# Performance work log

Hardware: AMD Instinct MI355X
Metric: run time of the kernel (lower is better)

Reference implementation:

```python
import jax, jax.numpy as jnp
import numpy as np

B, C, H, W, K = 32, 256, 56, 56, 4


def setup_inputs() -> dict:
    key = jax.random.key(0)
    k0, k1, k2, k3, k4 = jax.random.split(key, 5)
    return {
        "x0": jax.random.normal(k0, (B, C, H, W), dtype=jnp.float32),
        "x1": jax.random.normal(k1, (B, C, H, W), dtype=jnp.float32),
        "x2": jax.random.normal(k2, (B, C, H, W), dtype=jnp.float32),
        "x3": jax.random.normal(k3, (B, C, H, W), dtype=jnp.float32),
        "attn_logits": jax.random.normal(k4, (K, B, C), dtype=jnp.float32),
    }


def reference(x0, x1, x2, x3, attn_logits):
    # Stack K branches: [K, B, C, H, W]
    xs = jnp.stack([x0, x1, x2, x3], axis=0)
    # Op (1): U = sum over branches, S = global average pool over H,W -> [B, C]
    u = xs.sum(axis=0)                      # [B, C, H, W]
    s = u.mean(axis=(2, 3))                 # [B, C]
    # Op (2): per-(b,c) softmax over the K branch logits, then weighted fuse
    w = jax.nn.softmax(attn_logits, axis=0)  # [K, B, C]
    out = jnp.einsum("kbc,kbchw->bchw", w, xs)  # [B, C, H, W]
    # u_sum (HW-sum of U) as written by the fused kernel when write_usum=true
    u_sum = u.sum(axis=(2, 3))              # [B, C]
    return out, s, u_sum
```

## Files before the change

### kernel.cpp

```cpp
#include <hip/hip_runtime.h>

constexpr int B = 32, C = 256, H = 56, W = 56, K = 4;
constexpr int HW = H * W;
constexpr int BC = B * C;
constexpr long long IMG = (long long)BC * HW;

typedef float f4 __attribute__((ext_vector_type(4)));

__global__ __launch_bounds__(256) void sk_fuse_kernel(
    const float* __restrict__ x0, const float* __restrict__ x1,
    const float* __restrict__ x2, const float* __restrict__ x3,
    const float* __restrict__ logits,
    float* __restrict__ out,
    float* __restrict__ s_out,
    float* __restrict__ usum_out)
{
    const int bc  = blockIdx.x;
    const int tid = threadIdx.x;

    const float l0 = logits[0 * BC + bc];
    const float l1 = logits[1 * BC + bc];
    const float l2 = logits[2 * BC + bc];
    const float l3 = logits[3 * BC + bc];
    const float m  = fmaxf(fmaxf(l0, l1), fmaxf(l2, l3));
    const float e0 = expf(l0 - m);
    const float e1 = expf(l1 - m);
    const float e2 = expf(l2 - m);
    const float e3 = expf(l3 - m);
    const float inv = 1.0f / (e0 + e1 + e2 + e3);
    const float w0 = e0 * inv, w1 = e1 * inv, w2 = e2 * inv, w3 = e3 * inv;

    const size_t base = (size_t)bc * HW;
    const f4* __restrict__ p0 = (const f4*)(x0 + base);
    const f4* __restrict__ p1 = (const f4*)(x1 + base);
    const f4* __restrict__ p2 = (const f4*)(x2 + base);
    const f4* __restrict__ p3 = (const f4*)(x3 + base);
    f4* __restrict__ po = (f4*)(out + base);

    const int i0 = tid, i1 = tid + 256, i2 = tid + 512;
    const f4 a0 = p0[i0], b0 = p1[i0], c0 = p2[i0], d0 = p3[i0];
    const f4 a1 = p0[i1], b1 = p1[i1], c1 = p2[i1], d1 = p3[i1];
    const f4 a2 = p0[i2], b2 = p1[i2], c2 = p2[i2], d2 = p3[i2];

    const bool tail = (tid < 16);
    const int i3 = 768 + (tid & 15);
    f4 a3 = 0.0f, b3 = 0.0f, c3 = 0.0f, d3 = 0.0f;
    if (tail) { a3 = p0[i3]; b3 = p1[i3]; c3 = p2[i3]; d3 = p3[i3]; }

    float usum = 0.0f;

    auto fuse = [&](const f4& a, const f4& b,
                    const f4& c, const f4& d) -> f4 {
        f4 o;
        o.x = w0 * a.x + w1 * b.x + w2 * c.x + w3 * d.x;
        o.y = w0 * a.y + w1 * b.y + w2 * c.y + w3 * d.y;
        o.z = w0 * a.z + w1 * b.z + w2 * c.z + w3 * d.z;
        o.w = w0 * a.w + w1 * b.w + w2 * c.w + w3 * d.w;
        usum += (a.x + b.x + c.x + d.x)
              + (a.y + b.y + c.y + d.y)
              + (a.z + b.z + c.z + d.z)
              + (a.w + b.w + c.w + d.w);
        return o;
    };

    {
        const f4 o = fuse(a0, b0, c0, d0);
        __builtin_nontemporal_store(o, &po[i0]);
    }
    {
        const f4 o = fuse(a1, b1, c1, d1);
        __builtin_nontemporal_store(o, &po[i1]);
    }
    {
        const f4 o = fuse(a2, b2, c2, d2);
        __builtin_nontemporal_store(o, &po[i2]);
    }
    if (tail) {
        const f4 o = fuse(a3, b3, c3, d3);
        __builtin_nontemporal_store(o, &po[i3]);
    }

    #pragma unroll
    for (int off = 32; off > 0; off >>= 1)
        usum += __shfl_down(usum, off, 64);

    __shared__ float wsum[4];
    const int lane = tid & 63;
    const int wid  = tid >> 6;
    if (lane == 0) wsum[wid] = usum;
    __syncthreads();
    if (tid == 0) {
        const float t = wsum[0] + wsum[1] + wsum[2] + wsum[3];
        usum_out[bc] = t;
        s_out[bc]    = t * (1.0f / HW);
    }
}

extern "C" void kernel_launch(void* const* d_in, const int* in_sizes, int n_in,
                              void* d_out, int out_size, void* d_ws, size_t ws_size,
                              hipStream_t stream) {
    const float* x0     = (const float*)d_in[0];
    const float* x1     = (const float*)d_in[1];
    const float* x2     = (const float*)d_in[2];
    const float* x3     = (const float*)d_in[3];
    const float* logits = (const float*)d_in[4];

    float* out      = (float*)d_out;
    float* s_out    = out + IMG;
    float* usum_out = s_out + BC;

    sk_fuse_kernel<<<BC, 256, 0, stream>>>(x0, x1, x2, x3, logits,
                                           out, s_out, usum_out);
}
```

Measured before the change: 94.41 us.

## Process four planes per block with double-buffered register prefetch

Each block now handles four (b,c) planes instead of one. The loads for the next plane are issued into a second register buffer while the current plane is fused and stored, and the four reductions share a single shared-memory pass. The aim is to keep more memory requests in flight per thread and to spread per-block setup over more work. In exchange it uses more VGPRs (two 16-f4 buffers), which may lower occupancy, and it launches only 2048 blocks.

```diff
diff --git a/kernel.cpp b/kernel.cpp
--- a/kernel.cpp
+++ b/kernel.cpp
@@ -4,8 +4,57 @@
 constexpr int HW = H * W;
 constexpr int BC = B * C;
 constexpr long long IMG = (long long)BC * HW;
+constexpr int NP = 4;
 
 typedef float f4 __attribute__((ext_vector_type(4)));
+
+struct PlaneRegs { f4 v[16]; };
+
+__device__ __forceinline__ void issue_loads(
+    PlaneRegs& R,
+    const f4* __restrict__ p0, const f4* __restrict__ p1,
+    const f4* __restrict__ p2, const f4* __restrict__ p3,
+    int i0, int i1, int i2, int i3, bool tail)
+{
+    R.v[ 0] = p0[i0]; R.v[ 1] = p1[i0]; R.v[ 2] = p2[i0]; R.v[ 3] = p3[i0];
+    R.v[ 4] = p0[i1]; R.v[ 5] = p1[i1]; R.v[ 6] = p2[i1]; R.v[ 7] = p3[i1];
+    R.v[ 8] = p0[i2]; R.v[ 9] = p1[i2]; R.v[10] = p2[i2]; R.v[11] = p3[i2];
+    if (tail) {
+        R.v[12] = p0[i3]; R.v[13] = p1[i3]; R.v[14] = p2[i3]; R.v[15] = p3[i3];
+    } else {
+        R.v[12] = 0.0f; R.v[13] = 0.0f; R.v[14] = 0.0f; R.v[15] = 0.0f;
+    }
+}
+
+__device__ __forceinline__ f4 fuse1(const f4& a, const f4& b,
+                                    const f4& c, const f4& d,
+                                    float w0, float w1, float w2, float w3,
+                                    float& usum)
+{
+    f4 o;
+    o.x = w0 * a.x + w1 * b.x + w2 * c.x + w3 * d.x;
+    o.y = w0 * a.y + w1 * b.y + w2 * c.y + w3 * d.y;
+    o.z = w0 * a.z + w1 * b.z + w2 * c.z + w3 * d.z;
+    o.w = w0 * a.w + w1 * b.w + w2 * c.w + w3 * d.w;
+    usum += (a.x + b.x + c.x + d.x)
+          + (a.y + b.y + c.y + d.y)
+          + (a.z + b.z + c.z + d.z)
+          + (a.w + b.w + c.w + d.w);
+    return o;
+}
+
+__device__ __forceinline__ float consume(
+    const PlaneRegs& R, float w0, float w1, float w2, float w3,
+    f4* __restrict__ po, int i0, int i1, int i2, int i3, bool tail)
+{
+    float us = 0.0f;
+    __builtin_nontemporal_store(fuse1(R.v[0],R.v[1],R.v[ 2],R.v[ 3],w0,w1,w2,w3,us), &po[i0]);
+    __builtin_nontemporal_store(fuse1(R.v[4],R.v[5],R.v[ 6],R.v[ 7],w0,w1,w2,w3,us), &po[i1]);
+    __builtin_nontemporal_store(fuse1(R.v[8],R.v[9],R.v[10],R.v[11],w0,w1,w2,w3,us), &po[i2]);
+    if (tail)
+        __builtin_nontemporal_store(fuse1(R.v[12],R.v[13],R.v[14],R.v[15],w0,w1,w2,w3,us), &po[i3]);
+    return us;
+}
 
 __global__ __launch_bounds__(256) void sk_fuse_kernel(
     const float* __restrict__ x0, const float* __restrict__ x1,
@@ -15,84 +64,73 @@
     float* __restrict__ s_out,
     float* __restrict__ usum_out)
 {
-    const int bc  = blockIdx.x;
     const int tid = threadIdx.x;
-
-    const float l0 = logits[0 * BC + bc];
-    const float l1 = logits[1 * BC + bc];
-    const float l2 = logits[2 * BC + bc];
-    const float l3 = logits[3 * BC + bc];
-    const float m  = fmaxf(fmaxf(l0, l1), fmaxf(l2, l3));
-    const float e0 = expf(l0 - m);
-    const float e1 = expf(l1 - m);
-    const float e2 = expf(l2 - m);
-    const float e3 = expf(l3 - m);
-    const float inv = 1.0f / (e0 + e1 + e2 + e3);
-    const float w0 = e0 * inv, w1 = e1 * inv, w2 = e2 * inv, w3 = e3 * inv;
-
-    const size_t base = (size_t)bc * HW;
-    const f4* __restrict__ p0 = (const f4*)(x0 + base);
-    const f4* __restrict__ p1 = (const f4*)(x1 + base);
-    const f4* __restrict__ p2 = (const f4*)(x2 + base);
-    const f4* __restrict__ p3 = (const f4*)(x3 + base);
-    f4* __restrict__ po = (f4*)(out + base);
+    const int bc0 = blockIdx.x * NP;
 
     const int i0 = tid, i1 = tid + 256, i2 = tid + 512;
-    const f4 a0 = p0[i0], b0 = p1[i0], c0 = p2[i0], d0 = p3[i0];
-    const f4 a1 = p0[i1], b1 = p1[i1], c1 = p2[i1], d1 = p3[i1];
-    const f4 a2 = p0[i2], b2 = p1[i2], c2 = p2[i2], d2 = p3[i2];
-
     const bool tail = (tid < 16);
     const int i3 = 768 + (tid & 15);
-    f4 a3 = 0.0f, b3 = 0.0f, c3 = 0.0f, d3 = 0.0f;
-    if (tail) { a3 = p0[i3]; b3 = p1[i3]; c3 = p2[i3]; d3 = p3[i3]; }
 
-    float usum = 0.0f;
+    float w0[NP], w1[NP], w2[NP], w3[NP];
+    #pragma unroll
+    for (int q = 0; q < NP; ++q) {
+        const int bc = bc0 + q;
+        const float l0 = logits[0 * BC + bc];
+        const float l1 = logits[1 * BC + bc];
+        const float l2 = logits[2 * BC + bc];
+        const float l3 = logits[3 * BC + bc];
+        const float m  = fmaxf(fmaxf(l0, l1), fmaxf(l2, l3));
+        const float e0 = expf(l0 - m);
+        const float e1 = expf(l1 - m);
+        const float e2 = expf(l2 - m);
+        const float e3 = expf(l3 - m);
+        const float inv = 1.0f / (e0 + e1 + e2 + e3);
+        w0[q] = e0 * inv; w1[q] = e1 * inv; w2[q] = e2 * inv; w3[q] = e3 * inv;
+    }
 
-    auto fuse = [&](const f4& a, const f4& b,
-                    const f4& c, const f4& d) -> f4 {
-        f4 o;
-        o.x = w0 * a.x + w1 * b.x + w2 * c.x + w3 * d.x;
-        o.y = w0 * a.y + w1 * b.y + w2 * c.y + w3 * d.y;
-        o.z = w0 * a.z + w1 * b.z + w2 * c.z + w3 * d.z;
-        o.w = w0 * a.w + w1 * b.w + w2 * c.w + w3 * d.w;
-        usum += (a.x + b.x + c.x + d.x)
-              + (a.y + b.y + c.y + d.y)
-              + (a.z + b.z + c.z + d.z)
-              + (a.w + b.w + c.w + d.w);
-        return o;
-    };
+    PlaneRegs A, Bf;
+    float us[NP];
 
     {
-        const f4 o = fuse(a0, b0, c0, d0);
-        __builtin_nontemporal_store(o, &po[i0]);
-    }
-    {
-        const f4 o = fuse(a1, b1, c1, d1);
-        __builtin_nontemporal_store(o, &po[i1]);
-    }
-    {
-        const f4 o = fuse(a2, b2, c2, d2);
-        __builtin_nontemporal_store(o, &po[i2]);
-    }
-    if (tail) {
-        const f4 o = fuse(a3, b3, c3, d3);
-        __builtin_nontemporal_store(o, &po[i3]);
+        const size_t base = (size_t)bc0 * HW;
+        issue_loads(A, (const f4*)(x0 + base), (const f4*)(x1 + base),
+                       (const f4*)(x2 + base), (const f4*)(x3 + base),
+                    i0, i1, i2, i3, tail);
     }
 
     #pragma unroll
-    for (int off = 32; off > 0; off >>= 1)
-        usum += __shfl_down(usum, off, 64);
+    for (int q = 0; q < NP; ++q) {
+        PlaneRegs& cur = (q & 1) ? Bf : A;
+        PlaneRegs& nxt = (q & 1) ? A  : Bf;
+        if (q + 1 < NP) {
+            const size_t base = (size_t)(bc0 + q + 1) * HW;
+            issue_loads(nxt, (const f4*)(x0 + base), (const f4*)(x1 + base),
+                             (const f4*)(x2 + base), (const f4*)(x3 + base),
+                        i0, i1, i2, i3, tail);
+        }
+        f4* __restrict__ po = (f4*)(out + (size_t)(bc0 + q) * HW);
+        us[q] = consume(cur, w0[q], w1[q], w2[q], w3[q], po, i0, i1, i2, i3, tail);
+    }
 
-    __shared__ float wsum[4];
+    #pragma unroll
+    for (int off = 32; off > 0; off >>= 1) {
+        #pragma unroll
+        for (int q = 0; q < NP; ++q)
+            us[q] += __shfl_down(us[q], off, 64);
+    }
+
+    __shared__ float wsum[4][NP];
     const int lane = tid & 63;
     const int wid  = tid >> 6;
-    if (lane == 0) wsum[wid] = usum;
+    if (lane == 0) {
+        #pragma unroll
+        for (int q = 0; q < NP; ++q) wsum[wid][q] = us[q];
+    }
     __syncthreads();
-    if (tid == 0) {
-        const float t = wsum[0] + wsum[1] + wsum[2] + wsum[3];
-        usum_out[bc] = t;
-        s_out[bc]    = t * (1.0f / HW);
+    if (tid < NP) {
+        const float t = wsum[0][tid] + wsum[1][tid] + wsum[2][tid] + wsum[3][tid];
+        usum_out[bc0 + tid] = t;
+        s_out[bc0 + tid]    = t * (1.0f / HW);
     }
 }
 
@@ -109,6 +147,6 @@
     float* s_out    = out + IMG;
     float* usum_out = s_out + BC;
 
-    sk_fuse_kernel<<<BC, 256, 0, stream>>>(x0, x1, x2, x3, logits,
-                                           out, s_out, usum_out);
+    sk_fuse_kernel<<<BC / NP, 256, 0, stream>>>(x0, x1, x2, x3, logits,
+                                                out, s_out, usum_out);
 }
```

New measurement: 98.63 us. 1.04x slower.

## Process four bc planes per block with a smaller persistent-style grid

Applied to the files above, without the earlier changes.

Shrinks the grid from one block per (b,c) plane to 2048 blocks, each handling four planes strided by the grid size, with scheduling barriers between planes and one batched reduction at the end. It also sets a launch-bounds occupancy hint of 8 blocks per CU. The aim is to cut block launch and teardown overhead and amortise the final sync and reduction. In exchange each block does serialized work, so there may be fewer loads in flight per block and a risk of tail imbalance.

```diff
diff --git a/kernel.cpp b/kernel.cpp
--- a/kernel.cpp
+++ b/kernel.cpp
@@ -4,10 +4,12 @@
 constexpr int HW = H * W;
 constexpr int BC = B * C;
 constexpr long long IMG = (long long)BC * HW;
+constexpr int GRID = 2048;
+constexpr int NQ = BC / GRID;
 
 typedef float f4 __attribute__((ext_vector_type(4)));
 
-__global__ __launch_bounds__(256) void sk_fuse_kernel(
+__global__ __launch_bounds__(256, 8) void sk_fuse_kernel(
     const float* __restrict__ x0, const float* __restrict__ x1,
     const float* __restrict__ x2, const float* __restrict__ x3,
     const float* __restrict__ logits,
@@ -15,82 +17,88 @@
     float* __restrict__ s_out,
     float* __restrict__ usum_out)
 {
-    const int bc  = blockIdx.x;
     const int tid = threadIdx.x;
-
-    const float l0 = logits[0 * BC + bc];
-    const float l1 = logits[1 * BC + bc];
-    const float l2 = logits[2 * BC + bc];
-    const float l3 = logits[3 * BC + bc];
-    const float m  = fmaxf(fmaxf(l0, l1), fmaxf(l2, l3));
-    const float e0 = expf(l0 - m);
-    const float e1 = expf(l1 - m);
-    const float e2 = expf(l2 - m);
-    const float e3 = expf(l3 - m);
-    const float inv = 1.0f / (e0 + e1 + e2 + e3);
-    const float w0 = e0 * inv, w1 = e1 * inv, w2 = e2 * inv, w3 = e3 * inv;
-
-    const size_t base = (size_t)bc * HW;
-    const f4* __restrict__ p0 = (const f4*)(x0 + base);
-    const f4* __restrict__ p1 = (const f4*)(x1 + base);
-    const f4* __restrict__ p2 = (const f4*)(x2 + base);
-    const f4* __restrict__ p3 = (const f4*)(x3 + base);
-    f4* __restrict__ po = (f4*)(out + base);
-
     const int i0 = tid, i1 = tid + 256, i2 = tid + 512;
-    const f4 a0 = p0[i0], b0 = p1[i0], c0 = p2[i0], d0 = p3[i0];
-    const f4 a1 = p0[i1], b1 = p1[i1], c1 = p2[i1], d1 = p3[i1];
-    const f4 a2 = p0[i2], b2 = p1[i2], c2 = p2[i2], d2 = p3[i2];
-
     const bool tail = (tid < 16);
     const int i3 = 768 + (tid & 15);
-    f4 a3 = 0.0f, b3 = 0.0f, c3 = 0.0f, d3 = 0.0f;
-    if (tail) { a3 = p0[i3]; b3 = p1[i3]; c3 = p2[i3]; d3 = p3[i3]; }
 
-    float usum = 0.0f;
+    auto doPlane = [&](int bc) -> float {
+        const size_t base = (size_t)bc * HW;
+        const f4* __restrict__ p0 = (const f4*)(x0 + base);
+        const f4* __restrict__ p1 = (const f4*)(x1 + base);
+        const f4* __restrict__ p2 = (const f4*)(x2 + base);
+        const f4* __restrict__ p3 = (const f4*)(x3 + base);
+        f4* __restrict__ po = (f4*)(out + base);
 
-    auto fuse = [&](const f4& a, const f4& b,
-                    const f4& c, const f4& d) -> f4 {
-        f4 o;
-        o.x = w0 * a.x + w1 * b.x + w2 * c.x + w3 * d.x;
-        o.y = w0 * a.y + w1 * b.y + w2 * c.y + w3 * d.y;
-        o.z = w0 * a.z + w1 * b.z + w2 * c.z + w3 * d.z;
-        o.w = w0 * a.w + w1 * b.w + w2 * c.w + w3 * d.w;
-        usum += (a.x + b.x + c.x + d.x)
-              + (a.y + b.y + c.y + d.y)
-              + (a.z + b.z + c.z + d.z)
-              + (a.w + b.w + c.w + d.w);
-        return o;
+        const f4 a0 = p0[i0], b0 = p1[i0], c0 = p2[i0], d0 = p3[i0];
+        const f4 a1 = p0[i1], b1 = p1[i1], c1 = p2[i1], d1 = p3[i1];
+        const f4 a2 = p0[i2], b2 = p1[i2], c2 = p2[i2], d2 = p3[i2];
+        f4 a3 = 0.0f, b3 = 0.0f, c3 = 0.0f, d3 = 0.0f;
+        if (tail) { a3 = p0[i3]; b3 = p1[i3]; c3 = p2[i3]; d3 = p3[i3]; }
+
+        const float l0 = logits[0 * BC + bc];
+        const float l1 = logits[1 * BC + bc];
+        const float l2 = logits[2 * BC + bc];
+        const float l3 = logits[3 * BC + bc];
+        const float m  = fmaxf(fmaxf(l0, l1), fmaxf(l2, l3));
+        const float e0 = expf(l0 - m);
+        const float e1 = expf(l1 - m);
+        const float e2 = expf(l2 - m);
+        const float e3 = expf(l3 - m);
+        const float inv = 1.0f / (e0 + e1 + e2 + e3);
+        const float w0 = e0 * inv, w1 = e1 * inv, w2 = e2 * inv, w3 = e3 * inv;
+
+        float us = 0.0f;
+        auto fuse = [&](const f4& a, const f4& b,
+                        const f4& c, const f4& d) -> f4 {
+            f4 o;
+            o.x = w0 * a.x + w1 * b.x + w2 * c.x + w3 * d.x;
+            o.y = w0 * a.y + w1 * b.y + w2 * c.y + w3 * d.y;
+            o.z = w0 * a.z + w1 * b.z + w2 * c.z + w3 * d.z;
+            o.w = w0 * a.w + w1 * b.w + w2 * c.w + w3 * d.w;
+            us += (a.x + b.x + c.x + d.x)
+                + (a.y + b.y + c.y + d.y)
+                + (a.z + b.z + c.z + d.z)
+                + (a.w + b.w + c.w + d.w);
+            return o;
+        };
+
+        __builtin_nontemporal_store(fuse(a0, b0, c0, d0), &po[i0]);
+        __builtin_nontemporal_store(fuse(a1, b1, c1, d1), &po[i1]);
+        __builtin_nontemporal_store(fuse(a2, b2, c2, d2), &po[i2]);
+        if (tail)
+            __builtin_nontemporal_store(fuse(a3, b3, c3, d3), &po[i3]);
+        return us;
     };
 
-    {
-        const f4 o = fuse(a0, b0, c0, d0);
-        __builtin_nontemporal_store(o, &po[i0]);
-    }
-    {
-        const f4 o = fuse(a1, b1, c1, d1);
-        __builtin_nontemporal_store(o, &po[i1]);
-    }
-    {
-        const f4 o = fuse(a2, b2, c2, d2);
-        __builtin_nontemporal_store(o, &po[i2]);
-    }
-    if (tail) {
-        const f4 o = fuse(a3, b3, c3, d3);
-        __builtin_nontemporal_store(o, &po[i3]);
+    const float us0 = doPlane(blockIdx.x + 0 * GRID);
+    __builtin_amdgcn_sched_barrier(0);
+    const float us1 = doPlane(blockIdx.x + 1 * GRID);
+    __builtin_amdgcn_sched_barrier(0);
+    const float us2 = doPlane(blockIdx.x + 2 * GRID);
+    __builtin_amdgcn_sched_barrier(0);
+    const float us3 = doPlane(blockIdx.x + 3 * GRID);
+
+    float r0 = us0, r1 = us1, r2 = us2, r3 = us3;
+    #pragma unroll
+    for (int off = 32; off > 0; off >>= 1) {
+        r0 += __shfl_down(r0, off, 64);
+        r1 += __shfl_down(r1, off, 64);
+        r2 += __shfl_down(r2, off, 64);
+        r3 += __shfl_down(r3, off, 64);
     }
 
-    #pragma unroll
-    for (int off = 32; off > 0; off >>= 1)
-        usum += __shfl_down(usum, off, 64);
-
-    __shared__ float wsum[4];
+    __shared__ float wsum[4][NQ];
     const int lane = tid & 63;
     const int wid  = tid >> 6;
-    if (lane == 0) wsum[wid] = usum;
+    if (lane == 0) {
+        wsum[wid][0] = r0; wsum[wid][1] = r1;
+        wsum[wid][2] = r2; wsum[wid][3] = r3;
+    }
     __syncthreads();
-    if (tid == 0) {
-        const float t = wsum[0] + wsum[1] + wsum[2] + wsum[3];
+    if (tid < NQ) {
+        const int bc = blockIdx.x + tid * GRID;
+        const float t = wsum[0][tid] + wsum[1][tid] + wsum[2][tid] + wsum[3][tid];
         usum_out[bc] = t;
         s_out[bc]    = t * (1.0f / HW);
     }
@@ -109,6 +117,6 @@
     float* s_out    = out + IMG;
     float* usum_out = s_out + BC;
 
-    sk_fuse_kernel<<<BC, 256, 0, stream>>>(x0, x1, x2, x3, logits,
-                                           out, s_out, usum_out);
+    sk_fuse_kernel<<<GRID, 256, 0, stream>>>(x0, x1, x2, x3, logits,
+                                             out, s_out, usum_out);
 }
```

New measurement: 137.9 us (median of 5 runs). +46.1%, slower.
